# Optimization experiments

Hardware: AMD Instinct MI355X
Metric: run time of the kernel (lower is better)

Reference implementation:

```python
import jax, jax.numpy as jnp
import numpy as np

LATENT_DIM = 64
HIDDEN_DIM = 256
N_STEPS = 32  # fixed-step RK4 stand-in for adaptive dopri5 over t: 1.0 -> 0.0
BATCH = 16384


def setup_inputs() -> dict:
    key = jax.random.key(0)
    ks = jax.random.split(key, 5)
    D, H, B = LATENT_DIM, HIDDEN_DIM, BATCH
    u = lambda k, shape: jax.random.uniform(k, shape, jnp.float32, -0.01, 0.01)
    return {
        "z": jax.random.normal(ks[0], (B, D), jnp.float32),
        "W1": u(ks[1], (H, D)), "b1": jnp.zeros((H,), jnp.float32),
        "W2": u(ks[2], (H, H)), "b2": jnp.zeros((H,), jnp.float32),
        "W3": u(ks[3], (H, H)), "b3": jnp.zeros((H,), jnp.float32),
        "W4": u(ks[4], (D, H)), "b4": jnp.zeros((D,), jnp.float32),
    }


def _mlp(params, z):
    W1, b1, W2, b2, W3, b3, W4, b4 = params
    h = jnp.tanh(z @ W1.T + b1)
    h = jnp.tanh(h @ W2.T + b2)
    h = jnp.tanh(h @ W3.T + b3)
    return h @ W4.T + b4


def _aug_dyn(params, states):
    # states: [B, D+1] = [z, logp]
    z = states[:, :LATENT_DIM]
    dz = _mlp(params, z)
    # exact divergence = trace of Jacobian of the MLP (fused forward-mode,
    # replacing the O(D) autograd loop in the torch code -- same math)
    jac = jax.vmap(jax.jacfwd(lambda x: _mlp(params, x)))(z)  # [B, D, D]
    div = jnp.einsum('bii->b', jac)
    return jnp.concatenate([dz, -div[:, None]], axis=1)


def _integrate(params, states0):
    dt = jnp.float32(-1.0 / N_STEPS)  # integrate t from 1.0 down to 0.0

    def step(s, _):
        k1 = _aug_dyn(params, s)
        k2 = _aug_dyn(params, s + 0.5 * dt * k1)
        k3 = _aug_dyn(params, s + 0.5 * dt * k2)
        k4 = _aug_dyn(params, s + dt * k3)
        return s + (dt / 6.0) * (k1 + 2.0 * k2 + 2.0 * k3 + k4), None

    s, _ = jax.lax.scan(step, states0, None, length=N_STEPS)
    return s


def reference(z, W1, b1, W2, b2, W3, b3, W4, b4):
    params = (W1, b1, W2, b2, W3, b3, W4, b4)
    B = z.shape[0]
    states0 = jnp.concatenate([z, jnp.zeros((B, 1), z.dtype)], axis=1)
    final = _integrate(params, states0)
    output = final[:, :LATENT_DIM]
    log_prob = final[:, LATENT_DIM]
    return output, log_prob
```

## Files before the change

### kernel.cpp

```cpp
#include <hip/hip_runtime.h>

#define NSAMP 16384
#define NSTEP 32

typedef __attribute__((ext_vector_type(8))) short bf16x8;
typedef __attribute__((ext_vector_type(4))) short short4v;
typedef __attribute__((ext_vector_type(4))) float f32x4;
typedef __attribute__((ext_vector_type(2))) unsigned int uint2v;
typedef __attribute__((ext_vector_type(4))) unsigned int uint4v;

__device__ __forceinline__ unsigned short f2bf(float f) {
    unsigned int u = __float_as_uint(f);
    u += 0x7FFFu + ((u >> 16) & 1u);
    return (unsigned short)(u >> 16);
}
__device__ __forceinline__ float bf2fs(short h) {
    return __uint_as_float(((unsigned int)(unsigned short)h) << 16);
}
__device__ __forceinline__ unsigned int cvtpk(float a, float b) {
    unsigned int r;
    asm("v_cvt_pk_bf16_f32 %0, %1, %2" : "=v"(r) : "v"(a), "v"(b));
    return r;
}
__device__ __forceinline__ float ftanh(float x) {
    float e = __expf(2.0f * x);
    return 1.0f - __fdividef(2.0f, e + 1.0f);
}

__global__ void prep_kernel(const float* __restrict__ W1, const float* __restrict__ W2,
                            const float* __restrict__ W3, const float* __restrict__ W4,
                            unsigned short* __restrict__ ws) {
    int j = blockIdx.x * blockDim.x + threadIdx.x;
    if (j < 65536) {
        int e = j & 7, l = (j >> 3) & 63, s = (j >> 9) & 1, ks = (j >> 10) & 7, w = j >> 13;
        int m = (w << 5) + (s << 4) + (l & 15);
        int k = (ks << 5) + ((l >> 4) << 3) + e;
        ws[j]         = f2bf(W2[m * 256 + k]);
        ws[65536 + j] = f2bf(W3[m * 256 + k]);
    }
    if (j < 16384) {
        int i = j >> 8, k = j & 255;
        ws[131072 + j] = f2bf(W1[k * 64 + i]);
        ws[147456 + j] = f2bf(W4[j]);
        int e = j & 7, l = (j >> 3) & 63, ms = (j >> 9) & 1, ks = (j >> 10) & 1, w = j >> 11;
        int m = (w << 5) + (ms << 4) + (l & 15);
        int i2 = (ks << 5) + ((l >> 4) << 3) + e;
        ws[163840 + j] = f2bf(W1[m * 64 + i2]);
    }
}


#define ZERO5()                                                              \
    _Pragma("unroll") for (int ms = 0; ms < 2; ++ms)                         \
    _Pragma("unroll") for (int ns = 0; ns < 5; ++ns)                         \
        acc[ms][ns] = (f32x4){0.f, 0.f, 0.f, 0.f};

#define ZERO4()                                                              \
    _Pragma("unroll") for (int ms = 0; ms < 2; ++ms)                         \
    _Pragma("unroll") for (int ns = 0; ns < 4; ++ns)                         \
        acc[ms][ns] = (f32x4){0.f, 0.f, 0.f, 0.f};

#define GEMM_PASS_A(WF, HBASE)                                               \
    __builtin_amdgcn_s_setprio(1);                                           \
    _Pragma("unroll") for (int ks = 0; ks < 8; ++ks) {                       \
        const int kr = (ks << 5) + kband;                                    \
        bf16x8 bfr[5];                                                       \
        _Pragma("unroll") for (int ns = 0; ns < 4; ++ns)                     \
            bfr[ns] = *(const bf16x8*)&XT[((ns << 4) + lm) * 264 + kr];      \
        bfr[4] = *(const bf16x8*)&XT[(HBASE + (lm & 1)) * 264 + kr];         \
        _Pragma("unroll") for (int ms = 0; ms < 2; ++ms)                     \
        _Pragma("unroll") for (int ns = 0; ns < 5; ++ns)                     \
            acc[ms][ns] = __builtin_amdgcn_mfma_f32_16x16x32_bf16(           \
                WF[ks][ms], bfr[ns], acc[ms][ns], 0, 0, 0);                  \
    }                                                                        \
    __builtin_amdgcn_s_setprio(0);

#define GEMM_PASS_B(WF)                                                      \
    __builtin_amdgcn_s_setprio(1);                                           \
    _Pragma("unroll") for (int ks = 0; ks < 8; ++ks) {                       \
        const int kr = (ks << 5) + kband;                                    \
        bf16x8 bfr[4];                                                       \
        _Pragma("unroll") for (int ns = 0; ns < 4; ++ns)                     \
            bfr[ns] = *(const bf16x8*)&XT[(((ns + 4) << 4) + lm) * 264 + kr];\
        _Pragma("unroll") for (int ms = 0; ms < 2; ++ms)                     \
        _Pragma("unroll") for (int ns = 0; ns < 4; ++ns)                     \
            acc[ms][ns] = __builtin_amdgcn_mfma_f32_16x16x32_bf16(           \
                WF[ks][ms], bfr[ns], acc[ms][ns], 0, 0, 0);                  \
    }                                                                        \
    __builtin_amdgcn_s_setprio(0);

#define BUILD_SLICE(S)                                                       \
    {                                                                        \
        _Pragma("unroll") for (int c = 0; c < 4; ++c) {                      \
            const int kk = kcol0 + (c << 3);                                 \
            const bf16x8 wv = *(const bf16x8*)&W1T[l * 264 + kk];            \
            const float4 d0 = *(const float4*)&dvec1[(S)*256 + kk];          \
            const float4 d1_ = *(const float4*)&dvec1[(S)*256 + kk + 4];     \
            uint4v o;                                                        \
            o[0] = cvtpk(bf2fs(wv[0]) * d0.x, bf2fs(wv[1]) * d0.y);          \
            o[1] = cvtpk(bf2fs(wv[2]) * d0.z, bf2fs(wv[3]) * d0.w);          \
            o[2] = cvtpk(bf2fs(wv[4]) * d1_.x, bf2fs(wv[5]) * d1_.y);        \
            o[3] = cvtpk(bf2fs(wv[6]) * d1_.z, bf2fs(wv[7]) * d1_.w);        \
            *(uint4v*)&XT[((S)*64 + l) * 264 + kk] = o;                      \
        }                                                                    \
    }

__launch_bounds__(512, 2)
__global__ void cnf_kernel(const float* __restrict__ zin,
                           const float* __restrict__ b1g, const float* __restrict__ b2g,
                           const float* __restrict__ b3g, const float* __restrict__ b4g,
                           const unsigned short* __restrict__ ws,
                           float* __restrict__ out)
{
    __shared__ __align__(16) unsigned short XT[132 * 264];
    __shared__ __align__(16) unsigned short W1T[64 * 264];
    __shared__ __align__(16) unsigned short W4L[64 * 264];
    __shared__ __align__(16) unsigned short ZBT[16 * 72];
    __shared__ __align__(16) float dvec1[2 * 256];
    __shared__ __align__(16) float d2vec[2 * 256];
    __shared__ __align__(16) float d3vec[2 * 256];
    __shared__ __align__(16) float hvec[2 * 256];
    __shared__ __align__(16) float b1l[256], b2l[256], b3l[256], b4l[64];
    __shared__ __align__(16) float zbv[2 * 64];
    __shared__ __align__(16) float kav[2 * 64];
    __shared__ float wredp[16];
    __shared__ float misc[4];

    const int tid = threadIdx.x;
    const int w = tid >> 6;
    const int l = tid & 63;
    const int lm = l & 15;
    const int bid = blockIdx.x;
    const int r0 = (w << 5) + ((l >> 4) << 2);
    const int kband = (l >> 4) << 3;
    const int kcol0 = w << 5;
    const float DT = -1.0f / 32.0f;

    bf16x8 w2f[8][2], w3f[8][2], w1f[2][2];
    {
        const bf16x8* w2g = (const bf16x8*)ws;
        const bf16x8* w3g = w2g + 8192;
        const bf16x8* w1g = (const bf16x8*)(ws + 163840);
#pragma unroll
        for (int ks = 0; ks < 8; ++ks)
#pragma unroll
            for (int s = 0; s < 2; ++s) {
                int idx = (((w << 3) + ks) * 2 + s) * 64 + l;
                w2f[ks][s] = w2g[idx];
                w3f[ks][s] = w3g[idx];
            }
#pragma unroll
        for (int ks = 0; ks < 2; ++ks)
#pragma unroll
            for (int ms = 0; ms < 2; ++ms)
                w1f[ks][ms] = w1g[(((w << 1) + ks) * 2 + ms) * 64 + l];
    }
    for (int c = tid; c < 2048; c += 512) {
        int i = c >> 5, k0 = (c & 31) << 3;
        *(bf16x8*)&W1T[i * 264 + k0] = *(const bf16x8*)&ws[131072 + i * 256 + k0];
        *(bf16x8*)&W4L[i * 264 + k0] = *(const bf16x8*)&ws[147456 + i * 256 + k0];
    }
    for (int c = 144 + tid; c < 1152; c += 512) ZBT[c] = 0;
    for (int c = tid; c < 256; c += 512) { b1l[c] = b1g[c]; b2l[c] = b2g[c]; b3l[c] = b3g[c]; }
    if (tid < 128) {
        const int s = tid >> 6, i = tid & 63;
        if (s == 0) b4l[i] = b4g[i];
        float z = zin[(bid * 2 + s) * 64 + i];
        zbv[tid] = z;
        ZBT[s * 72 + i] = f2bf(z);
    }
    if (tid < 2) { misc[tid] = 0.f; misc[2 + tid] = 0.f; }
    __syncthreads();

    for (int it = 0; it < NSTEP * 4; ++it) {
        const int e = it & 3;
        f32x4 acc[2][5];

        if (it > 0 && tid < 2) {
            const int ep = (it - 1) & 3;
            float div = 0.f;
#pragma unroll
            for (int q = 0; q < 8; ++q) div += wredp[tid * 8 + q];
            const float wgt = (ep == 0 || ep == 3) ? 1.f : 2.f;
            float kl = (ep == 0) ? -div : misc[tid] - wgt * div;
            misc[tid] = kl;
            if (ep == 3) misc[2 + tid] += (DT / 6.0f) * kl;
        }
        {
            f32x4 az[2];
            az[0] = (f32x4){0.f, 0.f, 0.f, 0.f};
            az[1] = (f32x4){0.f, 0.f, 0.f, 0.f};
#pragma unroll
            for (int ks = 0; ks < 2; ++ks) {
                const bf16x8 zf = *(const bf16x8*)&ZBT[lm * 72 + (ks << 5) + kband];
#pragma unroll
                for (int ms = 0; ms < 2; ++ms)
                    az[ms] = __builtin_amdgcn_mfma_f32_16x16x32_bf16(w1f[ks][ms], zf, az[ms], 0, 0, 0);
            }
#pragma unroll
            for (int ms = 0; ms < 2; ++ms) {
                const int rb = r0 + (ms << 4);
                float hh[4], dd[4];
#pragma unroll
                for (int rg = 0; rg < 4; ++rg) {
                    float h = ftanh(az[ms][rg] + b1l[rb + rg]);
                    hh[rg] = h; dd[rg] = 1.f - h * h;
                }
                if (lm < 2) {
                    *(float4*)&dvec1[lm * 256 + rb] = make_float4(dd[0], dd[1], dd[2], dd[3]);
                    uint2v hp; hp[0] = cvtpk(hh[0], hh[1]); hp[1] = cvtpk(hh[2], hh[3]);
                    *(uint2v*)&XT[(128 + lm) * 264 + rb] = hp;
                }
            }
        }
        BUILD_SLICE(0)
        __syncthreads();

        BUILD_SLICE(1)
        ZERO5();
        GEMM_PASS_A(w2f, 128)
        __syncthreads();

        {
#pragma unroll
            for (int ms = 0; ms < 2; ++ms) {
                const int rb = r0 + (ms << 4);
                float hh[4], dd[4];
#pragma unroll
                for (int rg = 0; rg < 4; ++rg) {
                    float h = ftanh(acc[ms][4][rg] + b2l[rb + rg]);
                    hh[rg] = h; dd[rg] = 1.f - h * h;
                }
                if (lm < 2) {
                    uint2v hp; hp[0] = cvtpk(hh[0], hh[1]); hp[1] = cvtpk(hh[2], hh[3]);
                    *(uint2v*)&XT[(130 + lm) * 264 + rb] = hp;
                    *(float4*)&d2vec[lm * 256 + rb] = make_float4(dd[0], dd[1], dd[2], dd[3]);
                }
            }
#pragma unroll
            for (int ms = 0; ms < 2; ++ms) {
                const int rb = r0 + (ms << 4);
                const float4 ds = *(const float4*)&d2vec[rb];
#pragma unroll
                for (int ns = 0; ns < 4; ++ns) {
                    uint2v o;
                    o[0] = cvtpk(acc[ms][ns][0] * ds.x, acc[ms][ns][1] * ds.y);
                    o[1] = cvtpk(acc[ms][ns][2] * ds.z, acc[ms][ns][3] * ds.w);
                    *(uint2v*)&XT[((ns << 4) + lm) * 264 + rb] = o;
                }
            }
            ZERO4();
            GEMM_PASS_B(w2f)
        }
        __syncthreads();

        {
#pragma unroll
            for (int ms = 0; ms < 2; ++ms) {
                const int rb = r0 + (ms << 4);
                const float4 ds = *(const float4*)&d2vec[256 + rb];
#pragma unroll
                for (int ns = 0; ns < 4; ++ns) {
                    uint2v o;
                    o[0] = cvtpk(acc[ms][ns][0] * ds.x, acc[ms][ns][1] * ds.y);
                    o[1] = cvtpk(acc[ms][ns][2] * ds.z, acc[ms][ns][3] * ds.w);
                    *(uint2v*)&XT[(((ns + 4) << 4) + lm) * 264 + rb] = o;
                }
            }
            ZERO5();
            GEMM_PASS_A(w3f, 130)
        }
        __syncthreads();

        float p0 = 0.f;
        {
#pragma unroll
            for (int ms = 0; ms < 2; ++ms) {
                const int rb = r0 + (ms << 4);
                float hh[4], dd[4];
#pragma unroll
                for (int rg = 0; rg < 4; ++rg) {
                    float h = ftanh(acc[ms][4][rg] + b3l[rb + rg]);
                    hh[rg] = h; dd[rg] = 1.f - h * h;
                }
                if (lm < 2) {
                    *(float4*)&hvec[lm * 256 + rb] = make_float4(hh[0], hh[1], hh[2], hh[3]);
                    *(float4*)&d3vec[lm * 256 + rb] = make_float4(dd[0], dd[1], dd[2], dd[3]);
                }
            }
#pragma unroll
            for (int ms = 0; ms < 2; ++ms) {
                const int rb = r0 + (ms << 4);
                const float4 ds = *(const float4*)&d3vec[rb];
#pragma unroll
                for (int ns = 0; ns < 4; ++ns) {
                    const short4v wv = *(const short4v*)&W4L[((ns << 4) + lm) * 264 + rb];
                    p0 += acc[ms][ns][0] * ds.x * bf2fs(wv[0]);
                    p0 += acc[ms][ns][1] * ds.y * bf2fs(wv[1]);
                    p0 += acc[ms][ns][2] * ds.z * bf2fs(wv[2]);
                    p0 += acc[ms][ns][3] * ds.w * bf2fs(wv[3]);
                }
            }
            ZERO4();
            GEMM_PASS_B(w3f)
        }
        __syncthreads();

        {
            float p1 = 0.f;
#pragma unroll
            for (int ms = 0; ms < 2; ++ms) {
                const int rb = r0 + (ms << 4);
                const float4 ds = *(const float4*)&d3vec[256 + rb];
#pragma unroll
                for (int ns = 0; ns < 4; ++ns) {
                    const short4v wv = *(const short4v*)&W4L[((ns << 4) + lm) * 264 + rb];
                    p1 += acc[ms][ns][0] * ds.x * bf2fs(wv[0]);
                    p1 += acc[ms][ns][1] * ds.y * bf2fs(wv[1]);
                    p1 += acc[ms][ns][2] * ds.z * bf2fs(wv[2]);
                    p1 += acc[ms][ns][3] * ds.w * bf2fs(wv[3]);
                }
            }
#pragma unroll
            for (int o = 32; o; o >>= 1) {
                p0 += __shfl_xor(p0, o, 64);
                p1 += __shfl_xor(p1, o, 64);
            }
            if (l == 0) { wredp[w] = p0; wredp[8 + w] = p1; }

            const int s = w >> 2, i0 = (w & 3) << 4, i = i0 + lm, ch = l >> 4;
            const unsigned short* wr = &W4L[i * 264 + (ch << 6)];
            const float* hv = &hvec[s * 256 + (ch << 6)];
            float a = 0.f;
#pragma unroll
            for (int c = 0; c < 8; ++c) {
                bf16x8 wv = *(const bf16x8*)&wr[c * 8];
                float4 h0 = *(const float4*)&hv[c * 8];
                float4 h1 = *(const float4*)&hv[c * 8 + 4];
                a += bf2fs(wv[0]) * h0.x + bf2fs(wv[1]) * h0.y + bf2fs(wv[2]) * h0.z + bf2fs(wv[3]) * h0.w;
                a += bf2fs(wv[4]) * h1.x + bf2fs(wv[5]) * h1.y + bf2fs(wv[6]) * h1.z + bf2fs(wv[7]) * h1.w;
            }
            a += __shfl_xor(a, 16, 64);
            a += __shfl_xor(a, 32, 64);
            const float dz = a + b4l[i];

            const float wgt = (e == 0 || e == 3) ? 1.f : 2.f;
            const float kv = (e == 0) ? dz : kav[s * 64 + i] + wgt * dz;
            float znew;
            if (e < 3) {
                const float cc = (e == 2) ? 1.0f : 0.5f;
                znew = zbv[s * 64 + i] + cc * DT * dz;
            } else {
                znew = zbv[s * 64 + i] + (DT / 6.0f) * kv;
            }
            if (l < 16) {
                kav[s * 64 + i] = kv;
                if (e == 3) zbv[s * 64 + i] = znew;
                ZBT[s * 72 + i] = f2bf(znew);
            }
        }
        __syncthreads();
    }

    if (tid < 2) {
        float div = 0.f;
#pragma unroll
        for (int q = 0; q < 8; ++q) div += wredp[tid * 8 + q];
        float kl = misc[tid] - div;
        misc[2 + tid] += (DT / 6.0f) * kl;
    }
    __syncthreads();

    if (tid < 128) {
        const int s = tid >> 6, i = tid & 63;
        out[(bid * 2 + s) * 64 + i] = zbv[tid];
        if (i == 0) out[NSAMP * 64 + bid * 2 + s] = misc[2 + s];
    }
}

extern "C" void kernel_launch(void* const* d_in, const int* in_sizes, int n_in,
                              void* d_out, int out_size, void* d_ws, size_t ws_size,
                              hipStream_t stream) {
    const float* z  = (const float*)d_in[0];
    const float* W1 = (const float*)d_in[1];
    const float* b1 = (const float*)d_in[2];
    const float* W2 = (const float*)d_in[3];
    const float* b2 = (const float*)d_in[4];
    const float* W3 = (const float*)d_in[5];
    const float* b3 = (const float*)d_in[6];
    const float* W4 = (const float*)d_in[7];
    const float* b4 = (const float*)d_in[8];
    unsigned short* ws = (unsigned short*)d_ws;
    float* out = (float*)d_out;

    hipLaunchKernelGGL(prep_kernel, dim3(256), dim3(256), 0, stream, W1, W2, W3, W4, ws);
    hipLaunchKernelGGL(cnf_kernel, dim3(NSAMP / 2), dim3(512), 0, stream, z, b1, b2, b3, b4, ws, out);
}
```

Baseline: 42.89 ms.

## Split work across 16 waves per block with half-size per-wave tiles

Doubles the block to 1024 threads so each wave owns 16 output rows of the hidden GEMMs instead of 32. This halves the per-wave weight fragments and accumulators, and the divergence-reduction and dz matvec paths are remapped to the new wave layout. The aim is more resident waves per CU, since LDS use already limits each CU to one block, so MFMA and LDS latency can be hidden better. The launch bound of (1024,4) asks for an occupancy the hardware cannot reach and may force a very low VGPR cap and spilling. Each block also now synchronises twice as many waves.

```diff
diff --git a/kernel.cpp b/kernel.cpp
--- a/kernel.cpp
+++ b/kernel.cpp
@@ -51,14 +51,12 @@
 
 
 #define ZERO5()                                                              \
-    _Pragma("unroll") for (int ms = 0; ms < 2; ++ms)                         \
     _Pragma("unroll") for (int ns = 0; ns < 5; ++ns)                         \
-        acc[ms][ns] = (f32x4){0.f, 0.f, 0.f, 0.f};
+        acc[ns] = (f32x4){0.f, 0.f, 0.f, 0.f};
 
 #define ZERO4()                                                              \
-    _Pragma("unroll") for (int ms = 0; ms < 2; ++ms)                         \
     _Pragma("unroll") for (int ns = 0; ns < 4; ++ns)                         \
-        acc[ms][ns] = (f32x4){0.f, 0.f, 0.f, 0.f};
+        acc[ns] = (f32x4){0.f, 0.f, 0.f, 0.f};
 
 #define GEMM_PASS_A(WF, HBASE)                                               \
     __builtin_amdgcn_s_setprio(1);                                           \
@@ -68,10 +66,9 @@
         _Pragma("unroll") for (int ns = 0; ns < 4; ++ns)                     \
             bfr[ns] = *(const bf16x8*)&XT[((ns << 4) + lm) * 264 + kr];      \
         bfr[4] = *(const bf16x8*)&XT[(HBASE + (lm & 1)) * 264 + kr];         \
-        _Pragma("unroll") for (int ms = 0; ms < 2; ++ms)                     \
         _Pragma("unroll") for (int ns = 0; ns < 5; ++ns)                     \
-            acc[ms][ns] = __builtin_amdgcn_mfma_f32_16x16x32_bf16(           \
-                WF[ks][ms], bfr[ns], acc[ms][ns], 0, 0, 0);                  \
+            acc[ns] = __builtin_amdgcn_mfma_f32_16x16x32_bf16(               \
+                WF[ks], bfr[ns], acc[ns], 0, 0, 0);                          \
     }                                                                        \
     __builtin_amdgcn_s_setprio(0);
 
@@ -82,16 +79,15 @@
         bf16x8 bfr[4];                                                       \
         _Pragma("unroll") for (int ns = 0; ns < 4; ++ns)                     \
             bfr[ns] = *(const bf16x8*)&XT[(((ns + 4) << 4) + lm) * 264 + kr];\
-        _Pragma("unroll") for (int ms = 0; ms < 2; ++ms)                     \
         _Pragma("unroll") for (int ns = 0; ns < 4; ++ns)                     \
-            acc[ms][ns] = __builtin_amdgcn_mfma_f32_16x16x32_bf16(           \
-                WF[ks][ms], bfr[ns], acc[ms][ns], 0, 0, 0);                  \
+            acc[ns] = __builtin_amdgcn_mfma_f32_16x16x32_bf16(               \
+                WF[ks], bfr[ns], acc[ns], 0, 0, 0);                          \
     }                                                                        \
     __builtin_amdgcn_s_setprio(0);
 
 #define BUILD_SLICE(S)                                                       \
     {                                                                        \
-        _Pragma("unroll") for (int c = 0; c < 4; ++c) {                      \
+        _Pragma("unroll") for (int c = 0; c < 2; ++c) {                      \
             const int kk = kcol0 + (c << 3);                                 \
             const bf16x8 wv = *(const bf16x8*)&W1T[l * 264 + kk];            \
             const float4 d0 = *(const float4*)&dvec1[(S)*256 + kk];          \
@@ -100,12 +96,12 @@
             o[0] = cvtpk(bf2fs(wv[0]) * d0.x, bf2fs(wv[1]) * d0.y);          \
             o[1] = cvtpk(bf2fs(wv[2]) * d0.z, bf2fs(wv[3]) * d0.w);          \
             o[2] = cvtpk(bf2fs(wv[4]) * d1_.x, bf2fs(wv[5]) * d1_.y);        \
-            o[3] = cvtpk(bf2fs(wv[6]) * d1_.z, bf2fs(wv[7]) * d1_.w);        \
+            o[3] = cvtpk(bf2fs(wv[6]) * d1_.z, bf2fs(wv[7]) * d1_.w);       \
             *(uint4v*)&XT[((S)*64 + l) * 264 + kk] = o;                      \
         }                                                                    \
     }
 
-__launch_bounds__(512, 2)
+__launch_bounds__(1024, 4)
 __global__ void cnf_kernel(const float* __restrict__ zin,
                            const float* __restrict__ b1g, const float* __restrict__ b2g,
                            const float* __restrict__ b3g, const float* __restrict__ b4g,
@@ -123,7 +119,7 @@
     __shared__ __align__(16) float b1l[256], b2l[256], b3l[256], b4l[64];
     __shared__ __align__(16) float zbv[2 * 64];
     __shared__ __align__(16) float kav[2 * 64];
-    __shared__ float wredp[16];
+    __shared__ float wredp[32];
     __shared__ float misc[4];
 
     const int tid = threadIdx.x;
@@ -131,37 +127,34 @@
     const int l = tid & 63;
     const int lm = l & 15;
     const int bid = blockIdx.x;
-    const int r0 = (w << 5) + ((l >> 4) << 2);
+    const int r0 = (w << 4) + ((l >> 4) << 2);
     const int kband = (l >> 4) << 3;
-    const int kcol0 = w << 5;
+    const int kcol0 = w << 4;
     const float DT = -1.0f / 32.0f;
 
-    bf16x8 w2f[8][2], w3f[8][2], w1f[2][2];
+    bf16x8 w2f[8], w3f[8], w1f[2];
     {
         const bf16x8* w2g = (const bf16x8*)ws;
         const bf16x8* w3g = w2g + 8192;
         const bf16x8* w1g = (const bf16x8*)(ws + 163840);
-#pragma unroll
-        for (int ks = 0; ks < 8; ++ks)
-#pragma unroll
-            for (int s = 0; s < 2; ++s) {
-                int idx = (((w << 3) + ks) * 2 + s) * 64 + l;
-                w2f[ks][s] = w2g[idx];
-                w3f[ks][s] = w3g[idx];
-            }
+        const int ow = w >> 1, sm = w & 1;
+#pragma unroll
+        for (int ks = 0; ks < 8; ++ks) {
+            int idx = (((ow << 3) + ks) * 2 + sm) * 64 + l;
+            w2f[ks] = w2g[idx];
+            w3f[ks] = w3g[idx];
+        }
 #pragma unroll
         for (int ks = 0; ks < 2; ++ks)
-#pragma unroll
-            for (int ms = 0; ms < 2; ++ms)
-                w1f[ks][ms] = w1g[(((w << 1) + ks) * 2 + ms) * 64 + l];
-    }
-    for (int c = tid; c < 2048; c += 512) {
+            w1f[ks] = w1g[(((ow << 1) + ks) * 2 + sm) * 64 + l];
+    }
+    for (int c = tid; c < 2048; c += 1024) {
         int i = c >> 5, k0 = (c & 31) << 3;
         *(bf16x8*)&W1T[i * 264 + k0] = *(const bf16x8*)&ws[131072 + i * 256 + k0];
         *(bf16x8*)&W4L[i * 264 + k0] = *(const bf16x8*)&ws[147456 + i * 256 + k0];
     }
-    for (int c = 144 + tid; c < 1152; c += 512) ZBT[c] = 0;
-    for (int c = tid; c < 256; c += 512) { b1l[c] = b1g[c]; b2l[c] = b2g[c]; b3l[c] = b3g[c]; }
+    for (int c = 144 + tid; c < 1152; c += 1024) ZBT[c] = 0;
+    if (tid < 256) { b1l[tid] = b1g[tid]; b2l[tid] = b2g[tid]; b3l[tid] = b3g[tid]; }
     if (tid < 128) {
         const int s = tid >> 6, i = tid & 63;
         if (s == 0) b4l[i] = b4g[i];
@@ -174,44 +167,36 @@
 
     for (int it = 0; it < NSTEP * 4; ++it) {
         const int e = it & 3;
-        f32x4 acc[2][5];
+        f32x4 acc[5];
 
         if (it > 0 && tid < 2) {
             const int ep = (it - 1) & 3;
             float div = 0.f;
 #pragma unroll
-            for (int q = 0; q < 8; ++q) div += wredp[tid * 8 + q];
+            for (int q = 0; q < 16; ++q) div += wredp[tid * 16 + q];
             const float wgt = (ep == 0 || ep == 3) ? 1.f : 2.f;
             float kl = (ep == 0) ? -div : misc[tid] - wgt * div;
             misc[tid] = kl;
             if (ep == 3) misc[2 + tid] += (DT / 6.0f) * kl;
         }
         {
-            f32x4 az[2];
-            az[0] = (f32x4){0.f, 0.f, 0.f, 0.f};
-            az[1] = (f32x4){0.f, 0.f, 0.f, 0.f};
+            f32x4 az = (f32x4){0.f, 0.f, 0.f, 0.f};
 #pragma unroll
             for (int ks = 0; ks < 2; ++ks) {
                 const bf16x8 zf = *(const bf16x8*)&ZBT[lm * 72 + (ks << 5) + kband];
-#pragma unroll
-                for (int ms = 0; ms < 2; ++ms)
-                    az[ms] = __builtin_amdgcn_mfma_f32_16x16x32_bf16(w1f[ks][ms], zf, az[ms], 0, 0, 0);
-            }
-#pragma unroll
-            for (int ms = 0; ms < 2; ++ms) {
-                const int rb = r0 + (ms << 4);
-                float hh[4], dd[4];
-#pragma unroll
-                for (int rg = 0; rg < 4; ++rg) {
-                    float h = ftanh(az[ms][rg] + b1l[rb + rg]);
-                    hh[rg] = h; dd[rg] = 1.f - h * h;
-                }
-                if (lm < 2) {
-                    *(float4*)&dvec1[lm * 256 + rb] = make_float4(dd[0], dd[1], dd[2], dd[3]);
-                    uint2v hp; hp[0] = cvtpk(hh[0], hh[1]); hp[1] = cvtpk(hh[2], hh[3]);
-                    *(uint2v*)&XT[(128 + lm) * 264 + rb] = hp;
-                }
-            }
+                az = __builtin_amdgcn_mfma_f32_16x16x32_bf16(w1f[ks], zf, az, 0, 0, 0);
+            }
+            float hh[4], dd[4];
+#pragma unroll
+            for (int rg = 0; rg < 4; ++rg) {
+                float h = ftanh(az[rg] + b1l[r0 + rg]);
+                hh[rg] = h; dd[rg] = 1.f - h * h;
+            }
+            if (lm < 2)
+                *(float4*)&dvec1[lm * 256 + r0] = make_float4(dd[0], dd[1], dd[2], dd[3]);
+            uint2v hp; hp[0] = cvtpk(hh[0], hh[1]); hp[1] = cvtpk(hh[2], hh[3]);
+            if (lm < 2)
+                *(uint2v*)&XT[(128 + lm) * 264 + r0] = hp;
         }
         BUILD_SLICE(0)
         __syncthreads();
@@ -222,32 +207,25 @@
         __syncthreads();
 
         {
-#pragma unroll
-            for (int ms = 0; ms < 2; ++ms) {
-                const int rb = r0 + (ms << 4);
-                float hh[4], dd[4];
-#pragma unroll
-                for (int rg = 0; rg < 4; ++rg) {
-                    float h = ftanh(acc[ms][4][rg] + b2l[rb + rg]);
-                    hh[rg] = h; dd[rg] = 1.f - h * h;
-                }
-                if (lm < 2) {
-                    uint2v hp; hp[0] = cvtpk(hh[0], hh[1]); hp[1] = cvtpk(hh[2], hh[3]);
-                    *(uint2v*)&XT[(130 + lm) * 264 + rb] = hp;
-                    *(float4*)&d2vec[lm * 256 + rb] = make_float4(dd[0], dd[1], dd[2], dd[3]);
-                }
-            }
-#pragma unroll
-            for (int ms = 0; ms < 2; ++ms) {
-                const int rb = r0 + (ms << 4);
-                const float4 ds = *(const float4*)&d2vec[rb];
-#pragma unroll
-                for (int ns = 0; ns < 4; ++ns) {
-                    uint2v o;
-                    o[0] = cvtpk(acc[ms][ns][0] * ds.x, acc[ms][ns][1] * ds.y);
-                    o[1] = cvtpk(acc[ms][ns][2] * ds.z, acc[ms][ns][3] * ds.w);
-                    *(uint2v*)&XT[((ns << 4) + lm) * 264 + rb] = o;
-                }
+            float hh[4], dd[4];
+#pragma unroll
+            for (int rg = 0; rg < 4; ++rg) {
+                float h = ftanh(acc[4][rg] + b2l[r0 + rg]);
+                hh[rg] = h; dd[rg] = 1.f - h * h;
+            }
+            if (lm < 2)
+                *(float4*)&d2vec[lm * 256 + r0] = make_float4(dd[0], dd[1], dd[2], dd[3]);
+            uint2v hp; hp[0] = cvtpk(hh[0], hh[1]); hp[1] = cvtpk(hh[2], hh[3]);
+            if (lm < 2)
+                *(uint2v*)&XT[(130 + lm) * 264 + r0] = hp;
+
+            const float4 ds = *(const float4*)&d2vec[r0];
+#pragma unroll
+            for (int ns = 0; ns < 4; ++ns) {
+                uint2v o;
+                o[0] = cvtpk(acc[ns][0] * ds.x, acc[ns][1] * ds.y);
+                o[1] = cvtpk(acc[ns][2] * ds.z, acc[ns][3] * ds.w);
+                *(uint2v*)&XT[((ns << 4) + lm) * 264 + r0] = o;
             }
             ZERO4();
             GEMM_PASS_B(w2f)
@@ -255,17 +233,13 @@
         __syncthreads();
 
         {
-#pragma unroll
-            for (int ms = 0; ms < 2; ++ms) {
-                const int rb = r0 + (ms << 4);
-                const float4 ds = *(const float4*)&d2vec[256 + rb];
-#pragma unroll
-                for (int ns = 0; ns < 4; ++ns) {
-                    uint2v o;
-                    o[0] = cvtpk(acc[ms][ns][0] * ds.x, acc[ms][ns][1] * ds.y);
-                    o[1] = cvtpk(acc[ms][ns][2] * ds.z, acc[ms][ns][3] * ds.w);
-                    *(uint2v*)&XT[(((ns + 4) << 4) + lm) * 264 + rb] = o;
-                }
+            const float4 ds = *(const float4*)&d2vec[256 + r0];
+#pragma unroll
+            for (int ns = 0; ns < 4; ++ns) {
+                uint2v o;
+                o[0] = cvtpk(acc[ns][0] * ds.x, acc[ns][1] * ds.y);
+                o[1] = cvtpk(acc[ns][2] * ds.z, acc[ns][3] * ds.w);
+                *(uint2v*)&XT[(((ns + 4) << 4) + lm) * 264 + r0] = o;
             }
             ZERO5();
             GEMM_PASS_A(w3f, 130)
@@ -274,32 +248,24 @@
 
         float p0 = 0.f;
         {
-#pragma unroll
-            for (int ms = 0; ms < 2; ++ms) {
-                const int rb = r0 + (ms << 4);
-                float hh[4], dd[4];
-#pragma unroll
-                for (int rg = 0; rg < 4; ++rg) {
-                    float h = ftanh(acc[ms][4][rg] + b3l[rb + rg]);
-                    hh[rg] = h; dd[rg] = 1.f - h * h;
-                }
-                if (lm < 2) {
-                    *(float4*)&hvec[lm * 256 + rb] = make_float4(hh[0], hh[1], hh[2], hh[3]);
-                    *(float4*)&d3vec[lm * 256 + rb] = make_float4(dd[0], dd[1], dd[2], dd[3]);
-                }
-            }
-#pragma unroll
-            for (int ms = 0; ms < 2; ++ms) {
-                const int rb = r0 + (ms << 4);
-                const float4 ds = *(const float4*)&d3vec[rb];
-#pragma unroll
-                for (int ns = 0; ns < 4; ++ns) {
-                    const short4v wv = *(const short4v*)&W4L[((ns << 4) + lm) * 264 + rb];
-                    p0 += acc[ms][ns][0] * ds.x * bf2fs(wv[0]);
-                    p0 += acc[ms][ns][1] * ds.y * bf2fs(wv[1]);
-                    p0 += acc[ms][ns][2] * ds.z * bf2fs(wv[2]);
-                    p0 += acc[ms][ns][3] * ds.w * bf2fs(wv[3]);
-                }
+            float hh[4], dd[4];
+#pragma unroll
+            for (int rg = 0; rg < 4; ++rg) {
+                float h = ftanh(acc[4][rg] + b3l[r0 + rg]);
+                hh[rg] = h; dd[rg] = 1.f - h * h;
+            }
+            if (lm < 2) {
+                *(float4*)&hvec[lm * 256 + r0] = make_float4(hh[0], hh[1], hh[2], hh[3]);
+                *(float4*)&d3vec[lm * 256 + r0] = make_float4(dd[0], dd[1], dd[2], dd[3]);
+            }
+            const float4 ds = *(const float4*)&d3vec[r0];
+#pragma unroll
+            for (int ns = 0; ns < 4; ++ns) {
+                const short4v wv = *(const short4v*)&W4L[((ns << 4) + lm) * 264 + r0];
+                p0 += acc[ns][0] * ds.x * bf2fs(wv[0]);
+                p0 += acc[ns][1] * ds.y * bf2fs(wv[1]);
+                p0 += acc[ns][2] * ds.z * bf2fs(wv[2]);
+                p0 += acc[ns][3] * ds.w * bf2fs(wv[3]);
             }
             ZERO4();
             GEMM_PASS_B(w3f)
@@ -308,38 +274,35 @@
 
         {
             float p1 = 0.f;
-#pragma unroll
-            for (int ms = 0; ms < 2; ++ms) {
-                const int rb = r0 + (ms << 4);
-                const float4 ds = *(const float4*)&d3vec[256 + rb];
-#pragma unroll
-                for (int ns = 0; ns < 4; ++ns) {
-                    const short4v wv = *(const short4v*)&W4L[((ns << 4) + lm) * 264 + rb];
-                    p1 += acc[ms][ns][0] * ds.x * bf2fs(wv[0]);
-                    p1 += acc[ms][ns][1] * ds.y * bf2fs(wv[1]);
-                    p1 += acc[ms][ns][2] * ds.z * bf2fs(wv[2]);
-                    p1 += acc[ms][ns][3] * ds.w * bf2fs(wv[3]);
-                }
+            const float4 ds = *(const float4*)&d3vec[256 + r0];
+#pragma unroll
+            for (int ns = 0; ns < 4; ++ns) {
+                const short4v wv = *(const short4v*)&W4L[((ns << 4) + lm) * 264 + r0];
+                p1 += acc[ns][0] * ds.x * bf2fs(wv[0]);
+                p1 += acc[ns][1] * ds.y * bf2fs(wv[1]);
+                p1 += acc[ns][2] * ds.z * bf2fs(wv[2]);
+                p1 += acc[ns][3] * ds.w * bf2fs(wv[3]);
             }
 #pragma unroll
             for (int o = 32; o; o >>= 1) {
                 p0 += __shfl_xor(p0, o, 64);
                 p1 += __shfl_xor(p1, o, 64);
             }
-            if (l == 0) { wredp[w] = p0; wredp[8 + w] = p1; }
-
-            const int s = w >> 2, i0 = (w & 3) << 4, i = i0 + lm, ch = l >> 4;
-            const unsigned short* wr = &W4L[i * 264 + (ch << 6)];
-            const float* hv = &hvec[s * 256 + (ch << 6)];
+            if (l == 0) { wredp[w] = p0; wredp[16 + w] = p1; }
+
+            const int s = w >> 3, i0 = (w & 7) << 3, i = i0 + (l & 7), ch = l >> 3;
+            const unsigned short* wr = &W4L[i * 264 + (ch << 5)];
+            const float* hv = &hvec[s * 256 + (ch << 5)];
             float a = 0.f;
 #pragma unroll
-            for (int c = 0; c < 8; ++c) {
+            for (int c = 0; c < 4; ++c) {
                 bf16x8 wv = *(const bf16x8*)&wr[c * 8];
                 float4 h0 = *(const float4*)&hv[c * 8];
                 float4 h1 = *(const float4*)&hv[c * 8 + 4];
                 a += bf2fs(wv[0]) * h0.x + bf2fs(wv[1]) * h0.y + bf2fs(wv[2]) * h0.z + bf2fs(wv[3]) * h0.w;
                 a += bf2fs(wv[4]) * h1.x + bf2fs(wv[5]) * h1.y + bf2fs(wv[6]) * h1.z + bf2fs(wv[7]) * h1.w;
             }
+            a += __shfl_xor(a, 8, 64);
             a += __shfl_xor(a, 16, 64);
             a += __shfl_xor(a, 32, 64);
             const float dz = a + b4l[i];
@@ -353,7 +316,7 @@
             } else {
                 znew = zbv[s * 64 + i] + (DT / 6.0f) * kv;
             }
-            if (l < 16) {
+            if (l < 8) {
                 kav[s * 64 + i] = kv;
                 if (e == 3) zbv[s * 64 + i] = znew;
                 ZBT[s * 72 + i] = f2bf(znew);
@@ -365,7 +328,7 @@
     if (tid < 2) {
         float div = 0.f;
 #pragma unroll
-        for (int q = 0; q < 8; ++q) div += wredp[tid * 8 + q];
+        for (int q = 0; q < 16; ++q) div += wredp[tid * 16 + q];
         float kl = misc[tid] - div;
         misc[2 + tid] += (DT / 6.0f) * kl;
     }
@@ -394,5 +357,5 @@
     float* out = (float*)d_out;
 
     hipLaunchKernelGGL(prep_kernel, dim3(256), dim3(256), 0, stream, W1, W2, W3, W4, ws);
-    hipLaunchKernelGGL(cnf_kernel, dim3(NSAMP / 2), dim3(512), 0, stream, z, b1, b2, b3, b4, ws, out);
-}
+    hipLaunchKernelGGL(cnf_kernel, dim3(NSAMP / 2), dim3(1024), 0, stream, z, b1, b2, b3, b4, ws, out);
+}
```

Result: slower. 57.72 ms (+34.6%).

## Shrink LDS footprint to double occupancy: bf16 vectors, global W1/W4, register state

Applied to the files above, without the earlier changes.

The W1T and W4L LDS copies are removed and read straight from the global workspace. The derivative and hidden vectors are stored as bf16 instead of fp32, and the per-sample z and k accumulators move from shared memory into registers. Launch bounds change from 2 to 4 blocks per CU, aiming at higher occupancy and better latency hiding. The cost is global/L2 reads on the W4 and W1 paths each stage, extra bf16 rounding of the tanh derivatives and hidden values, and tighter register pressure, since each block keeps its W2/W3 fragments resident in registers.

```diff
diff --git a/kernel.cpp b/kernel.cpp
--- a/kernel.cpp
+++ b/kernel.cpp
@@ -93,19 +93,18 @@
     {                                                                        \
         _Pragma("unroll") for (int c = 0; c < 4; ++c) {                      \
             const int kk = kcol0 + (c << 3);                                 \
-            const bf16x8 wv = *(const bf16x8*)&W1T[l * 264 + kk];            \
-            const float4 d0 = *(const float4*)&dvec1[(S)*256 + kk];          \
-            const float4 d1_ = *(const float4*)&dvec1[(S)*256 + kk + 4];     \
+            const bf16x8 wv = *(const bf16x8*)&wsW1T[l * 256 + kk];          \
+            const bf16x8 dv = *(const bf16x8*)&dvec1[(S)*256 + kk];          \
             uint4v o;                                                        \
-            o[0] = cvtpk(bf2fs(wv[0]) * d0.x, bf2fs(wv[1]) * d0.y);          \
-            o[1] = cvtpk(bf2fs(wv[2]) * d0.z, bf2fs(wv[3]) * d0.w);          \
-            o[2] = cvtpk(bf2fs(wv[4]) * d1_.x, bf2fs(wv[5]) * d1_.y);        \
-            o[3] = cvtpk(bf2fs(wv[6]) * d1_.z, bf2fs(wv[7]) * d1_.w);        \
+            o[0] = cvtpk(bf2fs(wv[0]) * bf2fs(dv[0]), bf2fs(wv[1]) * bf2fs(dv[1])); \
+            o[1] = cvtpk(bf2fs(wv[2]) * bf2fs(dv[2]), bf2fs(wv[3]) * bf2fs(dv[3])); \
+            o[2] = cvtpk(bf2fs(wv[4]) * bf2fs(dv[4]), bf2fs(wv[5]) * bf2fs(dv[5])); \
+            o[3] = cvtpk(bf2fs(wv[6]) * bf2fs(dv[6]), bf2fs(wv[7]) * bf2fs(dv[7])); \
             *(uint4v*)&XT[((S)*64 + l) * 264 + kk] = o;                      \
         }                                                                    \
     }
 
-__launch_bounds__(512, 2)
+__launch_bounds__(512, 4)
 __global__ void cnf_kernel(const float* __restrict__ zin,
                            const float* __restrict__ b1g, const float* __restrict__ b2g,
                            const float* __restrict__ b3g, const float* __restrict__ b4g,
@@ -113,16 +112,12 @@
                            float* __restrict__ out)
 {
     __shared__ __align__(16) unsigned short XT[132 * 264];
-    __shared__ __align__(16) unsigned short W1T[64 * 264];
-    __shared__ __align__(16) unsigned short W4L[64 * 264];
     __shared__ __align__(16) unsigned short ZBT[16 * 72];
-    __shared__ __align__(16) float dvec1[2 * 256];
-    __shared__ __align__(16) float d2vec[2 * 256];
-    __shared__ __align__(16) float d3vec[2 * 256];
-    __shared__ __align__(16) float hvec[2 * 256];
-    __shared__ __align__(16) float b1l[256], b2l[256], b3l[256], b4l[64];
-    __shared__ __align__(16) float zbv[2 * 64];
-    __shared__ __align__(16) float kav[2 * 64];
+    __shared__ __align__(16) unsigned short dvec1[2 * 256];
+    __shared__ __align__(16) unsigned short d2vec[2 * 256];
+    __shared__ __align__(16) unsigned short d3vec[2 * 256];
+    __shared__ __align__(16) unsigned short hvec[2 * 256];
+    __shared__ __align__(16) float b1l[256], b2l[256], b3l[256];
     __shared__ float wredp[16];
     __shared__ float misc[4];
 
@@ -136,6 +131,15 @@
     const int kcol0 = w << 5;
     const float DT = -1.0f / 32.0f;
 
+    const unsigned short* wsW1T = ws + 131072;
+    const unsigned short* wsW4  = ws + 147456;
+
+    const int sown = w >> 2;
+    const int iown = ((w & 3) << 4) + lm;
+    float b4r  = b4g[iown];
+    float zreg = zin[(bid * 2 + sown) * 64 + iown];
+    float kreg = 0.f;
+
     bf16x8 w2f[8][2], w3f[8][2], w1f[2][2];
     {
         const bf16x8* w2g = (const bf16x8*)ws;
@@ -155,19 +159,11 @@
             for (int ms = 0; ms < 2; ++ms)
                 w1f[ks][ms] = w1g[(((w << 1) + ks) * 2 + ms) * 64 + l];
     }
-    for (int c = tid; c < 2048; c += 512) {
-        int i = c >> 5, k0 = (c & 31) << 3;
-        *(bf16x8*)&W1T[i * 264 + k0] = *(const bf16x8*)&ws[131072 + i * 256 + k0];
-        *(bf16x8*)&W4L[i * 264 + k0] = *(const bf16x8*)&ws[147456 + i * 256 + k0];
-    }
     for (int c = 144 + tid; c < 1152; c += 512) ZBT[c] = 0;
     for (int c = tid; c < 256; c += 512) { b1l[c] = b1g[c]; b2l[c] = b2g[c]; b3l[c] = b3g[c]; }
     if (tid < 128) {
         const int s = tid >> 6, i = tid & 63;
-        if (s == 0) b4l[i] = b4g[i];
-        float z = zin[(bid * 2 + s) * 64 + i];
-        zbv[tid] = z;
-        ZBT[s * 72 + i] = f2bf(z);
+        ZBT[s * 72 + i] = f2bf(zin[(bid * 2 + s) * 64 + i]);
     }
     if (tid < 2) { misc[tid] = 0.f; misc[2 + tid] = 0.f; }
     __syncthreads();
@@ -207,7 +203,8 @@
                     hh[rg] = h; dd[rg] = 1.f - h * h;
                 }
                 if (lm < 2) {
-                    *(float4*)&dvec1[lm * 256 + rb] = make_float4(dd[0], dd[1], dd[2], dd[3]);
+                    uint2v dp; dp[0] = cvtpk(dd[0], dd[1]); dp[1] = cvtpk(dd[2], dd[3]);
+                    *(uint2v*)&dvec1[lm * 256 + rb] = dp;
                     uint2v hp; hp[0] = cvtpk(hh[0], hh[1]); hp[1] = cvtpk(hh[2], hh[3]);
                     *(uint2v*)&XT[(128 + lm) * 264 + rb] = hp;
                 }
@@ -232,20 +229,23 @@
                     hh[rg] = h; dd[rg] = 1.f - h * h;
                 }
                 if (lm < 2) {
+                    uint2v dp; dp[0] = cvtpk(dd[0], dd[1]); dp[1] = cvtpk(dd[2], dd[3]);
+                    *(uint2v*)&d2vec[lm * 256 + rb] = dp;
                     uint2v hp; hp[0] = cvtpk(hh[0], hh[1]); hp[1] = cvtpk(hh[2], hh[3]);
                     *(uint2v*)&XT[(130 + lm) * 264 + rb] = hp;
-                    *(float4*)&d2vec[lm * 256 + rb] = make_float4(dd[0], dd[1], dd[2], dd[3]);
-                }
-            }
-#pragma unroll
-            for (int ms = 0; ms < 2; ++ms) {
-                const int rb = r0 + (ms << 4);
-                const float4 ds = *(const float4*)&d2vec[rb];
+                }
+            }
+#pragma unroll
+            for (int ms = 0; ms < 2; ++ms) {
+                const int rb = r0 + (ms << 4);
+                const short4v dq = *(const short4v*)&d2vec[rb];
+                const float ds0 = bf2fs(dq[0]), ds1 = bf2fs(dq[1]);
+                const float ds2 = bf2fs(dq[2]), ds3 = bf2fs(dq[3]);
 #pragma unroll
                 for (int ns = 0; ns < 4; ++ns) {
                     uint2v o;
-                    o[0] = cvtpk(acc[ms][ns][0] * ds.x, acc[ms][ns][1] * ds.y);
-                    o[1] = cvtpk(acc[ms][ns][2] * ds.z, acc[ms][ns][3] * ds.w);
+                    o[0] = cvtpk(acc[ms][ns][0] * ds0, acc[ms][ns][1] * ds1);
+                    o[1] = cvtpk(acc[ms][ns][2] * ds2, acc[ms][ns][3] * ds3);
                     *(uint2v*)&XT[((ns << 4) + lm) * 264 + rb] = o;
                 }
             }
@@ -258,12 +258,14 @@
 #pragma unroll
             for (int ms = 0; ms < 2; ++ms) {
                 const int rb = r0 + (ms << 4);
-                const float4 ds = *(const float4*)&d2vec[256 + rb];
+                const short4v dq = *(const short4v*)&d2vec[256 + rb];
+                const float ds0 = bf2fs(dq[0]), ds1 = bf2fs(dq[1]);
+                const float ds2 = bf2fs(dq[2]), ds3 = bf2fs(dq[3]);
 #pragma unroll
                 for (int ns = 0; ns < 4; ++ns) {
                     uint2v o;
-                    o[0] = cvtpk(acc[ms][ns][0] * ds.x, acc[ms][ns][1] * ds.y);
-                    o[1] = cvtpk(acc[ms][ns][2] * ds.z, acc[ms][ns][3] * ds.w);
+                    o[0] = cvtpk(acc[ms][ns][0] * ds0, acc[ms][ns][1] * ds1);
+                    o[1] = cvtpk(acc[ms][ns][2] * ds2, acc[ms][ns][3] * ds3);
                     *(uint2v*)&XT[(((ns + 4) << 4) + lm) * 264 + rb] = o;
                 }
             }
@@ -284,21 +286,25 @@
                     hh[rg] = h; dd[rg] = 1.f - h * h;
                 }
                 if (lm < 2) {
-                    *(float4*)&hvec[lm * 256 + rb] = make_float4(hh[0], hh[1], hh[2], hh[3]);
-                    *(float4*)&d3vec[lm * 256 + rb] = make_float4(dd[0], dd[1], dd[2], dd[3]);
-                }
-            }
-#pragma unroll
-            for (int ms = 0; ms < 2; ++ms) {
-                const int rb = r0 + (ms << 4);
-                const float4 ds = *(const float4*)&d3vec[rb];
+                    uint2v hp; hp[0] = cvtpk(hh[0], hh[1]); hp[1] = cvtpk(hh[2], hh[3]);
+                    *(uint2v*)&hvec[lm * 256 + rb] = hp;
+                    uint2v dp; dp[0] = cvtpk(dd[0], dd[1]); dp[1] = cvtpk(dd[2], dd[3]);
+                    *(uint2v*)&d3vec[lm * 256 + rb] = dp;
+                }
+            }
+#pragma unroll
+            for (int ms = 0; ms < 2; ++ms) {
+                const int rb = r0 + (ms << 4);
+                const short4v dq = *(const short4v*)&d3vec[rb];
+                const float ds0 = bf2fs(dq[0]), ds1 = bf2fs(dq[1]);
+                const float ds2 = bf2fs(dq[2]), ds3 = bf2fs(dq[3]);
 #pragma unroll
                 for (int ns = 0; ns < 4; ++ns) {
-                    const short4v wv = *(const short4v*)&W4L[((ns << 4) + lm) * 264 + rb];
-                    p0 += acc[ms][ns][0] * ds.x * bf2fs(wv[0]);
-                    p0 += acc[ms][ns][1] * ds.y * bf2fs(wv[1]);
-                    p0 += acc[ms][ns][2] * ds.z * bf2fs(wv[2]);
-                    p0 += acc[ms][ns][3] * ds.w * bf2fs(wv[3]);
+                    const short4v wv = *(const short4v*)&wsW4[((ns << 4) + lm) * 256 + rb];
+                    p0 += acc[ms][ns][0] * ds0 * bf2fs(wv[0]);
+                    p0 += acc[ms][ns][1] * ds1 * bf2fs(wv[1]);
+                    p0 += acc[ms][ns][2] * ds2 * bf2fs(wv[2]);
+                    p0 += acc[ms][ns][3] * ds3 * bf2fs(wv[3]);
                 }
             }
             ZERO4();
@@ -311,14 +317,16 @@
 #pragma unroll
             for (int ms = 0; ms < 2; ++ms) {
                 const int rb = r0 + (ms << 4);
-                const float4 ds = *(const float4*)&d3vec[256 + rb];
+                const short4v dq = *(const short4v*)&d3vec[256 + rb];
+                const float ds0 = bf2fs(dq[0]), ds1 = bf2fs(dq[1]);
+                const float ds2 = bf2fs(dq[2]), ds3 = bf2fs(dq[3]);
 #pragma unroll
                 for (int ns = 0; ns < 4; ++ns) {
-                    const short4v wv = *(const short4v*)&W4L[((ns << 4) + lm) * 264 + rb];
-                    p1 += acc[ms][ns][0] * ds.x * bf2fs(wv[0]);
-                    p1 += acc[ms][ns][1] * ds.y * bf2fs(wv[1]);
-                    p1 += acc[ms][ns][2] * ds.z * bf2fs(wv[2]);
-                    p1 += acc[ms][ns][3] * ds.w * bf2fs(wv[3]);
+                    const short4v wv = *(const short4v*)&wsW4[((ns << 4) + lm) * 256 + rb];
+                    p1 += acc[ms][ns][0] * ds0 * bf2fs(wv[0]);
+                    p1 += acc[ms][ns][1] * ds1 * bf2fs(wv[1]);
+                    p1 += acc[ms][ns][2] * ds2 * bf2fs(wv[2]);
+                    p1 += acc[ms][ns][3] * ds3 * bf2fs(wv[3]);
                 }
             }
 #pragma unroll
@@ -328,53 +336,46 @@
             }
             if (l == 0) { wredp[w] = p0; wredp[8 + w] = p1; }
 
-            const int s = w >> 2, i0 = (w & 3) << 4, i = i0 + lm, ch = l >> 4;
-            const unsigned short* wr = &W4L[i * 264 + (ch << 6)];
-            const float* hv = &hvec[s * 256 + (ch << 6)];
+            const int ch = l >> 4;
+            const unsigned short* wr = wsW4 + iown * 256 + (ch << 6);
+            const unsigned short* hv = &hvec[sown * 256 + (ch << 6)];
             float a = 0.f;
 #pragma unroll
             for (int c = 0; c < 8; ++c) {
-                bf16x8 wv = *(const bf16x8*)&wr[c * 8];
-                float4 h0 = *(const float4*)&hv[c * 8];
-                float4 h1 = *(const float4*)&hv[c * 8 + 4];
-                a += bf2fs(wv[0]) * h0.x + bf2fs(wv[1]) * h0.y + bf2fs(wv[2]) * h0.z + bf2fs(wv[3]) * h0.w;
-                a += bf2fs(wv[4]) * h1.x + bf2fs(wv[5]) * h1.y + bf2fs(wv[6]) * h1.z + bf2fs(wv[7]) * h1.w;
+                const bf16x8 wv = *(const bf16x8*)&wr[c * 8];
+                const bf16x8 hb = *(const bf16x8*)&hv[c * 8];
+                a += bf2fs(wv[0]) * bf2fs(hb[0]) + bf2fs(wv[1]) * bf2fs(hb[1]);
+                a += bf2fs(wv[2]) * bf2fs(hb[2]) + bf2fs(wv[3]) * bf2fs(hb[3]);
+                a += bf2fs(wv[4]) * bf2fs(hb[4]) + bf2fs(wv[5]) * bf2fs(hb[5]);
+                a += bf2fs(wv[6]) * bf2fs(hb[6]) + bf2fs(wv[7]) * bf2fs(hb[7]);
             }
             a += __shfl_xor(a, 16, 64);
             a += __shfl_xor(a, 32, 64);
-            const float dz = a + b4l[i];
+            const float dz = a + b4r;
 
             const float wgt = (e == 0 || e == 3) ? 1.f : 2.f;
-            const float kv = (e == 0) ? dz : kav[s * 64 + i] + wgt * dz;
+            const float kv = (e == 0) ? dz : kreg + wgt * dz;
+            kreg = kv;
             float znew;
             if (e < 3) {
                 const float cc = (e == 2) ? 1.0f : 0.5f;
-                znew = zbv[s * 64 + i] + cc * DT * dz;
+                znew = zreg + cc * DT * dz;
             } else {
-                znew = zbv[s * 64 + i] + (DT / 6.0f) * kv;
-            }
-            if (l < 16) {
-                kav[s * 64 + i] = kv;
-                if (e == 3) zbv[s * 64 + i] = znew;
-                ZBT[s * 72 + i] = f2bf(znew);
-            }
-        }
-        __syncthreads();
-    }
-
+                znew = zreg + (DT / 6.0f) * kv;
+                zreg = znew;
+            }
+            if (l < 16) ZBT[sown * 72 + iown] = f2bf(znew);
+        }
+        __syncthreads();
+    }
+
+    if (l < 16) out[(bid * 2 + sown) * 64 + iown] = zreg;
     if (tid < 2) {
         float div = 0.f;
 #pragma unroll
         for (int q = 0; q < 8; ++q) div += wredp[tid * 8 + q];
         float kl = misc[tid] - div;
-        misc[2 + tid] += (DT / 6.0f) * kl;
-    }
-    __syncthreads();
-
-    if (tid < 128) {
-        const int s = tid >> 6, i = tid & 63;
-        out[(bid * 2 + s) * 64 + i] = zbv[tid];
-        if (i == 0) out[NSAMP * 64 + bid * 2 + s] = misc[2 + s];
+        out[NSAMP * 64 + bid * 2 + tid] = misc[2 + tid] + (DT / 6.0f) * kl;
     }
 }
 
```

After: 101.4 ms. 136% more time.
